# Kernel optimization log

Hardware: AMD Instinct MI355X
Metric: run time of the kernel (lower is better)

The kernel has to match this reference:

```python
import jax, jax.numpy as jnp
import numpy as np

EPS = 1e-5

def _bn(y, g, b):
    # BatchNorm1d training-mode math: biased batch stats over (batch, spatial)
    m = jnp.mean(y, axis=(0, 2), keepdims=True)
    v = jnp.var(y, axis=(0, 2), keepdims=True)
    return (y - m) / jnp.sqrt(v + EPS) * g[None, :, None] + b[None, :, None]

def setup_inputs() -> dict:
    key = jax.random.key(0)
    ks = jax.random.split(key, 8)
    B, C, HW = 32, 512, 1024
    D = C // 8
    s = 0.02
    return {
        "x": jax.random.normal(ks[0], (B, C, HW), dtype=jnp.float32),
        "bn1_g": jnp.ones((C,), jnp.float32),
        "bn1_b": jnp.zeros((C,), jnp.float32),
        "W_qkv": jax.random.normal(ks[1], (2 * D + C, C), jnp.float32) * s,
        "b_qkv": jnp.zeros((2 * D + C,), jnp.float32),
        "bn2_g": jnp.ones((C,), jnp.float32),
        "bn2_b": jnp.zeros((C,), jnp.float32),
        "W1": jax.random.normal(ks[2], (C, C), jnp.float32) * s,
        "b1": jnp.zeros((C,), jnp.float32),
        "W2": jax.random.normal(ks[3], (C, C), jnp.float32) * s,
        "b2": jnp.zeros((C,), jnp.float32),
    }

def reference(x, bn1_g, bn1_b, W_qkv, b_qkv, bn2_g, bn2_b, W1, b1, W2, b2):
    b, c, hw = x.shape
    d = c // 8
    h = jax.nn.relu(_bn(x, bn1_g, bn1_b))
    # 1x1 conv == channel matmul: [b, 2d+c, hw]
    qkv = jnp.einsum('oc,bch->boh', W_qkv, h) + b_qkv[None, :, None]
    q, k, v = qkv[:, :d], qkv[:, d:2 * d], qkv[:, 2 * d:]
    # beta[b, q_pos, k_pos]; note softmax over axis=1 (query axis), per original
    beta = jnp.einsum('bdq,bdk->bqk', q, k) / jnp.sqrt(jnp.asarray(d, x.dtype))
    beta = jax.nn.softmax(beta, axis=1)
    att = jnp.einsum('bcq,bqk->bck', v, beta)  # [b, c, hw]
    xr = x + att
    y = _bn(xr, bn2_g, bn2_b)
    y = jnp.transpose(y, (0, 2, 1))  # [b, hw, c]
    y = jax.nn.relu(y @ W1.T + b1) @ W2.T + b2
    return xr + jnp.transpose(y, (0, 2, 1))
```

## Files before the change

kernel.cpp:

```cpp
#include <hip/hip_runtime.h>

#define BB 32
#define CC 512
#define HWN 1024
#define DD 64
#define OO 640

typedef short bf16x8 __attribute__((ext_vector_type(8)));
typedef float f32x4 __attribute__((ext_vector_type(4)));
typedef __attribute__((address_space(1))) const void gvoid;
typedef __attribute__((address_space(3))) void svoid;

__device__ __forceinline__ void gload_lds16(const void* g, void* l) {
    __builtin_amdgcn_global_load_lds((gvoid*)g, (svoid*)l, 16, 0, 0);
}

__device__ __forceinline__ unsigned short f2bf(float f) {
    unsigned int u = __float_as_uint(f);
    unsigned int r = u + 0x7FFFu + ((u >> 16) & 1u);
    return (unsigned short)(r >> 16);
}
__device__ __forceinline__ float bf2f(unsigned short h) {
    return __uint_as_float(((unsigned int)h) << 16);
}

__global__ __launch_bounds__(256) void cvt3_kernel(const float* __restrict__ a,
                                                   const float* __restrict__ b,
                                                   const float* __restrict__ c,
                                                   unsigned short* __restrict__ oa,
                                                   unsigned short* __restrict__ ob,
                                                   unsigned short* __restrict__ oc) {
    const int n1 = OO * CC, n2 = CC * CC;
    int i = blockIdx.x * 256 + threadIdx.x;
    if (i < n1)            oa[i] = f2bf(a[i]);
    else if (i < n1 + n2)  ob[i - n1] = f2bf(b[i - n1]);
    else                   oc[i - n1 - n2] = f2bf(c[i - n1 - n2]);
}

template <bool INBF16>
__global__ __launch_bounds__(256) void bn_stats_kernel(const void* __restrict__ xv,
                                                       float* __restrict__ mean,
                                                       float* __restrict__ rstd) {
    int c = blockIdx.x;
    int t = threadIdx.x;
    float s = 0.f, s2 = 0.f;
    if (INBF16) {
        const unsigned int* x = (const unsigned int*)xv;
        for (int b = 0; b < BB; ++b) {
            const unsigned int* p = x + ((size_t)b * CC + c) * (HWN / 2);
#pragma unroll
            for (int i = 0; i < 2; ++i) {
                unsigned int w = p[t + i * 256];
                float v0 = bf2f((unsigned short)(w & 0xffffu));
                float v1 = bf2f((unsigned short)(w >> 16));
                s += v0 + v1; s2 += v0 * v0 + v1 * v1;
            }
        }
    } else {
        const float* x = (const float*)xv;
        for (int b = 0; b < BB; ++b) {
            const float* p = x + ((size_t)b * CC + c) * HWN;
#pragma unroll
            for (int i = 0; i < 4; ++i) {
                float v = p[t + i * 256];
                s += v; s2 += v * v;
            }
        }
    }
    for (int off = 32; off > 0; off >>= 1) {
        s  += __shfl_down(s,  off, 64);
        s2 += __shfl_down(s2, off, 64);
    }
    __shared__ float sh[4], sh2[4];
    int wave = t >> 6;
    if ((t & 63) == 0) { sh[wave] = s; sh2[wave] = s2; }
    __syncthreads();
    if (t == 0) {
        float ts = 0.f, ts2 = 0.f;
        for (int w = 0; w < 4; ++w) { ts += sh[w]; ts2 += sh2[w]; }
        const float invN = 1.f / (float)(BB * HWN);
        float m = ts * invN;
        float var = ts2 * invN - m * m;
        mean[c] = m;
        rstd[c] = rsqrtf(var + 1e-5f);
    }
}

template <bool RELU, bool INBF16>
__global__ __launch_bounds__(256) void bn_apply_t_kernel(const void* __restrict__ xv,
                                                         const float* __restrict__ mean,
                                                         const float* __restrict__ rstd,
                                                         const float* __restrict__ g,
                                                         const float* __restrict__ bta,
                                                         unsigned short* __restrict__ outT) {
    __shared__ float tile[64][65];
    int b  = blockIdx.z;
    int c0 = blockIdx.y * 64;
    int s0 = blockIdx.x * 64;
    int t = threadIdx.x;
    int sl = t & 63, grp = t >> 6;
#pragma unroll
    for (int i = 0; i < 16; ++i) {
        int cr = i * 4 + grp;
        int c = c0 + cr;
        float r  = rstd[c] * g[c];
        float sh = bta[c] - mean[c] * r;
        float xval;
        if (INBF16) {
            const unsigned short* xb = (const unsigned short*)xv;
            xval = bf2f(xb[((size_t)b * CC + c0 + cr) * HWN + s0 + sl]);
        } else {
            const float* xb = (const float*)xv;
            xval = xb[((size_t)b * CC + c0 + cr) * HWN + s0 + sl];
        }
        float v = fmaf(xval, r, sh);
        if (RELU) v = fmaxf(v, 0.f);
        tile[cr][sl] = v;
    }
    __syncthreads();
    unsigned short* ob = outT + ((size_t)b * HWN + s0) * CC + c0;
#pragma unroll
    for (int i = 0; i < 16; ++i) {
        int srow = i * 4 + grp;
        ob[(size_t)srow * CC + sl] = f2bf(tile[sl][srow]);
    }
}

__global__ __launch_bounds__(256) void reduce_bnstats_kernel(const float* __restrict__ part,
                                                             float* __restrict__ mean,
                                                             float* __restrict__ rstd) {
    int c = blockIdx.x * 256 + threadIdx.x;
    float s = 0.f, s2 = 0.f;
    for (int p = 0; p < BB * 8; ++p) {
        s  += part[(size_t)p * 1024 + c];
        s2 += part[(size_t)p * 1024 + 512 + c];
    }
    const float invN = 1.f / (float)(BB * HWN);
    float m = s * invN;
    mean[c] = m;
    rstd[c] = rsqrtf(s2 * invN - m * m + 1e-5f);
}

__global__ __launch_bounds__(512, 2) void fused_pv_kernel(
        const unsigned short* __restrict__ qkTg,
        const unsigned short* __restrict__ vg,
        const float* __restrict__ xg,
        unsigned short* __restrict__ xrg,
        float* __restrict__ rowpart) {
    __shared__ __align__(16) unsigned short Ks[2 * 128 * 32];
    __shared__ __align__(16) unsigned short Qs[2][2 * 64 * 32];
    __shared__ __align__(16) unsigned short Vs[2 * 512 * 32];
    __shared__ __align__(16) unsigned short Es[2 * 128 * 32];
    __shared__ float sS[128];
    __shared__ float rsS[2][512];
    __shared__ float rqS[2][512];

    int b = blockIdx.z;
    int n0 = blockIdx.x * 128;
    const unsigned short* qk = qkTg + (size_t)b * (HWN * 128);
    const unsigned short* vb = vg + (size_t)b * ((size_t)CC * HWN);
    int t = threadIdx.x;
    int wv = t >> 6, L = t & 63;
    int lr = L & 15, lq = L >> 4;
    int swz = (lr >> 1) & 3;
    int cstrip = (wv >> 1) * 128;
    int khalf = (wv & 1) * 64;

#pragma unroll
    for (int is = 0; is < 2; ++is) {
        int idx = is * 512 + t;
        int kkd = idx >> 9, row = (idx >> 2) & 127, slot = idx & 3;
        int ch = slot ^ ((row >> 1) & 3);
        gload_lds16(qk + (size_t)(n0 + row) * 128 + 64 + kkd * 32 + ch * 8, &Ks[idx * 8]);
    }
    {
        int kkd = t >> 8, row = (t >> 2) & 63, slot = t & 3;
        int ch = slot ^ ((row >> 1) & 3);
        gload_lds16(qk + (size_t)row * 128 + kkd * 32 + ch * 8, &Qs[0][t * 8]);
    }

    f32x4 acc[8][4] = {};
    float S = 0.f;
    int p = 0;
    for (int i = 0; i < 16; ++i) {
        int q0 = i * 64;
#pragma unroll
        for (int is = 0; is < 8; ++is) {
            int idx = is * 512 + t;
            int kkq = idx >> 11, row = (idx >> 2) & 511, slot = idx & 3;
            int ch = slot ^ ((row >> 1) & 3);
            gload_lds16(vb + (size_t)row * HWN + q0 + kkq * 32 + ch * 8, &Vs[idx * 8]);
        }
        if (i + 1 < 16) {
            int kkd = t >> 8, row = (t >> 2) & 63, slot = t & 3;
            int ch = slot ^ ((row >> 1) & 3);
            gload_lds16(qk + (size_t)(q0 + 64 + row) * 128 + kkd * 32 + ch * 8,
                        &Qs[p ^ 1][t * 8]);
        }
        if (i == 0) __syncthreads();

        f32x4 eacc[4] = {};
#pragma unroll
        for (int kkd = 0; kkd < 2; ++kkd) {
            bf16x8 kb = *(const bf16x8*)&Ks[kkd * 4096 + (wv * 16 + lr) * 32 + ((lq ^ swz) * 8)];
#pragma unroll
            for (int qi = 0; qi < 4; ++qi) {
                bf16x8 qa = *(const bf16x8*)&Qs[p][kkd * 2048 + (qi * 16 + lr) * 32 + ((lq ^ swz) * 8)];
                eacc[qi] = __builtin_amdgcn_mfma_f32_16x16x32_bf16(qa, kb, eacc[qi], 0, 0, 0);
            }
        }
        float spart = 0.f;
#pragma unroll
        for (int qi = 0; qi < 4; ++qi) {
            float e0 = __expf(eacc[qi][0] * 0.125f);
            float e1 = __expf(eacc[qi][1] * 0.125f);
            float e2 = __expf(eacc[qi][2] * 0.125f);
            float e3 = __expf(eacc[qi][3] * 0.125f);
            spart += (e0 + e1) + (e2 + e3);
            unsigned int lo = (unsigned int)f2bf(e0) | ((unsigned int)f2bf(e1) << 16);
            unsigned int hi = (unsigned int)f2bf(e2) | ((unsigned int)f2bf(e3) << 16);
            int kkq = qi >> 1;
            int chunkE = (qi & 1) * 2 + (lq >> 1);
            int addr = kkq * 4096 + (wv * 16 + lr) * 32 + ((chunkE ^ swz) * 8) + (lq & 1) * 4;
            *(uint2*)&Es[addr] = make_uint2(lo, hi);
        }
        spart += __shfl_xor(spart, 16, 64);
        spart += __shfl_xor(spart, 32, 64);
        S += spart;
        __syncthreads();

#pragma unroll
        for (int kk = 0; kk < 2; ++kk) {
            bf16x8 af[8], bfj[4];
#pragma unroll
            for (int ii = 0; ii < 8; ++ii)
                af[ii] = *(const bf16x8*)&Vs[kk * 16384 + (cstrip + ii * 16 + lr) * 32 + ((lq ^ swz) * 8)];
#pragma unroll
            for (int j = 0; j < 4; ++j)
                bfj[j] = *(const bf16x8*)&Es[kk * 4096 + (khalf + j * 16 + lr) * 32 + ((lq ^ swz) * 8)];
#pragma unroll
            for (int ii = 0; ii < 8; ++ii)
#pragma unroll
                for (int j = 0; j < 4; ++j)
                    acc[ii][j] = __builtin_amdgcn_mfma_f32_16x16x32_bf16(af[ii], bfj[j], acc[ii][j], 0, 0, 0);
        }
        __syncthreads();
        p ^= 1;
    }

    if (lq == 0) sS[wv * 16 + lr] = S;
    __syncthreads();
    float inv[4];
#pragma unroll
    for (int j = 0; j < 4; ++j) inv[j] = 1.f / sS[khalf + j * 16 + lr];

    const float* xb = xg + (size_t)b * ((size_t)CC * HWN);
    unsigned short* xrb = xrg + (size_t)b * ((size_t)CC * HWN);
#pragma unroll
    for (int ii = 0; ii < 8; ++ii) {
#pragma unroll
        for (int r = 0; r < 4; ++r) {
            int row = cstrip + ii * 16 + lq * 4 + r;
            float s = 0.f, q2 = 0.f;
#pragma unroll
            for (int j = 0; j < 4; ++j) {
                int col = n0 + khalf + j * 16 + lr;
                float val = acc[ii][j][r] * inv[j];
                size_t off = (size_t)row * HWN + col;
                val += xb[off];
                s += val; q2 += val * val;
                xrb[off] = f2bf(val);
            }
#pragma unroll
            for (int m = 1; m <= 8; m <<= 1) {
                s += __shfl_xor(s, m, 64);
                q2 += __shfl_xor(q2, m, 64);
            }
            if (lr == 0) { rsS[wv & 1][row] = s; rqS[wv & 1][row] = q2; }
        }
    }
    __syncthreads();
    {
        size_t base = ((size_t)b * 8 + blockIdx.x) * 1024;
        rowpart[base + t] = rsS[0][t] + rsS[1][t];
        rowpart[base + 512 + t] = rqS[0][t] + rqS[1][t];
    }
}

template <bool OUTBF16, int BIASMODE , bool RELU,
          int RESMODE >
__global__ __launch_bounds__(256, 4) void mfma_gemm(const unsigned short* __restrict__ A,
                                                 const unsigned short* __restrict__ Bt,
                                                 const float* __restrict__ bias,
                                                 const void* __restrict__ resid,
                                                 void* __restrict__ C,
                                                 int K, int lda, int ldb, int ldc,
                                                 long strideA, long strideB, long strideC,
                                                 float scale) {
    __shared__ __align__(16) unsigned short As[2][128 * 32];
    __shared__ __align__(16) unsigned short Bs[2][128 * 32];
    int b  = blockIdx.z;
    int m0 = blockIdx.y * 128;
    int n0 = blockIdx.x * 128;
    const unsigned short* Ab = A  + (size_t)b * strideA;
    const unsigned short* Bb = Bt + (size_t)b * strideB;
    int t = threadIdx.x;
    int wv = t >> 6, L = t & 63;
    int wm = (wv >> 1) * 64, wn = (wv & 1) * 64;
    int lr = L & 15, lq = L >> 4;
    int srow = t >> 2;
    int gchunk = (t & 3) ^ ((t >> 3) & 3);
    int skof = gchunk * 8;
    int swz = (lr >> 1) & 3;

    int aoff[4], boff[4];
#pragma unroll
    for (int i = 0; i < 4; ++i) {
        aoff[i] = (wm + i * 16 + lr) * 32 + ((lq ^ swz) * 8);
        boff[i] = (wn + i * 16 + lr) * 32 + ((lq ^ swz) * 8);
    }

    const unsigned short* gA0 = Ab + (size_t)(m0 + srow) * lda + skof;
    const unsigned short* gA1 = Ab + (size_t)(m0 + 64 + srow) * lda + skof;
    const unsigned short* gB0 = Bb + (size_t)(n0 + srow) * ldb + skof;
    const unsigned short* gB1 = Bb + (size_t)(n0 + 64 + srow) * ldb + skof;

    f32x4 acc[4][4] = {};
    int nIter = K >> 5;

    gload_lds16(gA0, &As[0][t * 8]);
    gload_lds16(gA1, &As[0][64 * 32 + t * 8]);
    gload_lds16(gB0, &Bs[0][t * 8]);
    gload_lds16(gB1, &Bs[0][64 * 32 + t * 8]);

    int p = 0;
    for (int i = 0; i < nIter; ++i) {
        __syncthreads();
        if (i + 1 < nIter) {
            int ko = (i + 1) << 5;
            gload_lds16(gA0 + ko, &As[p ^ 1][t * 8]);
            gload_lds16(gA1 + ko, &As[p ^ 1][64 * 32 + t * 8]);
            gload_lds16(gB0 + ko, &Bs[p ^ 1][t * 8]);
            gload_lds16(gB1 + ko, &Bs[p ^ 1][64 * 32 + t * 8]);
        }
        bf16x8 af[4], bfr[4];
#pragma unroll
        for (int j = 0; j < 4; ++j) af[j]  = *(const bf16x8*)&As[p][aoff[j]];
#pragma unroll
        for (int j = 0; j < 4; ++j) bfr[j] = *(const bf16x8*)&Bs[p][boff[j]];
#pragma unroll
        for (int ii = 0; ii < 4; ++ii)
#pragma unroll
            for (int jj = 0; jj < 4; ++jj)
                acc[ii][jj] = __builtin_amdgcn_mfma_f32_16x16x32_bf16(af[ii], bfr[jj], acc[ii][jj], 0, 0, 0);
        p ^= 1;
    }

#pragma unroll
    for (int i = 0; i < 4; ++i) {
#pragma unroll
        for (int r = 0; r < 4; ++r) {
            int row = m0 + wm + i * 16 + lq * 4 + r;
            float brow = (BIASMODE == 1) ? bias[row] : 0.f;
#pragma unroll
            for (int j = 0; j < 4; ++j) {
                int col = n0 + wn + j * 16 + lr;
                float v = acc[i][j][r] * scale;
                if (BIASMODE == 1) v += brow;
                if (BIASMODE == 2) v += bias[col];
                if (RELU) v = fmaxf(v, 0.f);
                size_t off = (size_t)b * strideC + (size_t)row * ldc + col;
                if (RESMODE == 1) v += ((const float*)resid)[off];
                if (RESMODE == 2) v += bf2f(((const unsigned short*)resid)[off]);
                if (OUTBF16) ((unsigned short*)C)[off] = f2bf(v);
                else         ((float*)C)[off] = v;
            }
        }
    }
}

extern "C" void kernel_launch(void* const* d_in, const int* in_sizes, int n_in,
                              void* d_out, int out_size, void* d_ws, size_t ws_size,
                              hipStream_t stream) {
    const float* x     = (const float*)d_in[0];
    const float* bn1_g = (const float*)d_in[1];
    const float* bn1_b = (const float*)d_in[2];
    const float* W_qkv = (const float*)d_in[3];
    const float* b_qkv = (const float*)d_in[4];
    const float* bn2_g = (const float*)d_in[5];
    const float* bn2_b = (const float*)d_in[6];
    const float* W1    = (const float*)d_in[7];
    const float* b1    = (const float*)d_in[8];
    const float* W2    = (const float*)d_in[9];
    const float* b2    = (const float*)d_in[10];
    float* out = (float*)d_out;
    char* ws = (char*)d_ws;

    unsigned short* hT    = (unsigned short*)(ws);
    unsigned short* qkT   = (unsigned short*)(ws + 33554432);
    unsigned short* v     = (unsigned short*)(ws + 41943040);
    unsigned short* xr    = (unsigned short*)(ws + 142606336);
    unsigned short* Wqkvb = (unsigned short*)(ws + 176160768);
    unsigned short* W1b   = (unsigned short*)(ws + 176816128);
    unsigned short* W2b   = (unsigned short*)(ws + 177340416);
    float* stats = (float*)(ws + 177864704);
    float* mean1 = stats,        *rstd1 = stats + 512;
    float* mean2 = stats + 1024, *rstd2 = stats + 1536;
    unsigned short* ybnT = hT;
    unsigned short* y1T  = v;
    float* rowpartBN = (float*)(ws + 1179648);

    const long sHT = (long)HWN * CC;
    const long sQK = (long)HWN * 128;
    const long sV  = (long)CC * HWN;

    cvt3_kernel<<<(OO * CC + 2 * CC * CC) / 256, 256, 0, stream>>>(W_qkv, W1, W2, Wqkvb, W1b, W2b);
    bn_stats_kernel<false><<<CC, 256, 0, stream>>>(x, mean1, rstd1);
    bn_apply_t_kernel<true, false><<<dim3(16, 8, BB), 256, 0, stream>>>(x, mean1, rstd1, bn1_g, bn1_b, hT);
    mfma_gemm<true, 2, false, 0><<<dim3(1, 8, BB), 256, 0, stream>>>(
        hT, Wqkvb, b_qkv, nullptr, qkT, 512, 512, 512, 128, sHT, 0, sQK, 1.f);
    mfma_gemm<true, 1, false, 0><<<dim3(8, 4, BB), 256, 0, stream>>>(
        Wqkvb + 128 * 512, hT, b_qkv + 128, nullptr, v, 512, 512, 512, 1024, 0, sHT, sV, 1.f);
    fused_pv_kernel<<<dim3(8, 1, BB), 512, 0, stream>>>(qkT, v, x, xr, rowpartBN);
    reduce_bnstats_kernel<<<2, 256, 0, stream>>>(rowpartBN, mean2, rstd2);
    bn_apply_t_kernel<false, true><<<dim3(16, 8, BB), 256, 0, stream>>>(xr, mean2, rstd2, bn2_g, bn2_b, ybnT);
    mfma_gemm<true, 2, true, 0><<<dim3(4, 8, BB), 256, 0, stream>>>(
        ybnT, W1b, b1, nullptr, y1T, 512, 512, 512, 512, sHT, 0, sHT, 1.f);
    mfma_gemm<false, 1, false, 2><<<dim3(8, 4, BB), 256, 0, stream>>>(
        W2b, y1T, b2, xr, out, 512, 512, 512, 1024, 0, sHT, sV, 1.f);
}
```

Before: 376.6 us.

## Split fused PV kernel over channel halves to double grid size and occupancy

The fused softmax-PV kernel now splits the 512 value channels into two 256-channel halves per block, doubling the grid from 256 to 512 blocks. This halves the V tile, the accumulator registers and the LDS footprint, and raises launch bounds to 4 blocks per CU. The Q tile is now single-buffered and its prefetch is issued after the barrier. In exchange, each half recomputes the QK^T exponentials, doubling that work, and it loses the overlap that double-buffered Q gave.

```diff
diff --git a/kernel.cpp b/kernel.cpp
--- a/kernel.cpp
+++ b/kernel.cpp
@@ -141,61 +141,58 @@
     rstd[c] = rsqrtf(s2 * invN - m * m + 1e-5f);
 }
 
-__global__ __launch_bounds__(512, 2) void fused_pv_kernel(
+__global__ __launch_bounds__(512, 4) void fused_pv_kernel(
         const unsigned short* __restrict__ qkTg,
         const unsigned short* __restrict__ vg,
         const float* __restrict__ xg,
         unsigned short* __restrict__ xrg,
         float* __restrict__ rowpart) {
     __shared__ __align__(16) unsigned short Ks[2 * 128 * 32];
-    __shared__ __align__(16) unsigned short Qs[2][2 * 64 * 32];
-    __shared__ __align__(16) unsigned short Vs[2 * 512 * 32];
+    __shared__ __align__(16) unsigned short Qs[2 * 64 * 32];
+    __shared__ __align__(16) unsigned short Vs[2 * 256 * 32];
     __shared__ __align__(16) unsigned short Es[2 * 128 * 32];
     __shared__ float sS[128];
-    __shared__ float rsS[2][512];
-    __shared__ float rqS[2][512];
-
-    int b = blockIdx.z;
-    int n0 = blockIdx.x * 128;
+    __shared__ float rsS[2][256];
+    __shared__ float rqS[2][256];
+
+    int lin = blockIdx.x + 16 * blockIdx.z;
+    int b  = lin & 31;
+    int nn = (lin >> 5) & 7;
+    int ch = lin >> 8;
+    int n0 = nn * 128;
+    int c0 = ch * 256;
     const unsigned short* qk = qkTg + (size_t)b * (HWN * 128);
     const unsigned short* vb = vg + (size_t)b * ((size_t)CC * HWN);
     int t = threadIdx.x;
     int wv = t >> 6, L = t & 63;
     int lr = L & 15, lq = L >> 4;
     int swz = (lr >> 1) & 3;
-    int cstrip = (wv >> 1) * 128;
+    int cstrip = (wv >> 1) * 64;
     int khalf = (wv & 1) * 64;
 
 #pragma unroll
     for (int is = 0; is < 2; ++is) {
         int idx = is * 512 + t;
         int kkd = idx >> 9, row = (idx >> 2) & 127, slot = idx & 3;
-        int ch = slot ^ ((row >> 1) & 3);
-        gload_lds16(qk + (size_t)(n0 + row) * 128 + 64 + kkd * 32 + ch * 8, &Ks[idx * 8]);
+        int chk = slot ^ ((row >> 1) & 3);
+        gload_lds16(qk + (size_t)(n0 + row) * 128 + 64 + kkd * 32 + chk * 8, &Ks[idx * 8]);
     }
     {
         int kkd = t >> 8, row = (t >> 2) & 63, slot = t & 3;
-        int ch = slot ^ ((row >> 1) & 3);
-        gload_lds16(qk + (size_t)row * 128 + kkd * 32 + ch * 8, &Qs[0][t * 8]);
-    }
-
-    f32x4 acc[8][4] = {};
+        int chk = slot ^ ((row >> 1) & 3);
+        gload_lds16(qk + (size_t)row * 128 + kkd * 32 + chk * 8, &Qs[t * 8]);
+    }
+
+    f32x4 acc[4][4] = {};
     float S = 0.f;
-    int p = 0;
     for (int i = 0; i < 16; ++i) {
         int q0 = i * 64;
 #pragma unroll
-        for (int is = 0; is < 8; ++is) {
+        for (int is = 0; is < 4; ++is) {
             int idx = is * 512 + t;
-            int kkq = idx >> 11, row = (idx >> 2) & 511, slot = idx & 3;
-            int ch = slot ^ ((row >> 1) & 3);
-            gload_lds16(vb + (size_t)row * HWN + q0 + kkq * 32 + ch * 8, &Vs[idx * 8]);
-        }
-        if (i + 1 < 16) {
-            int kkd = t >> 8, row = (t >> 2) & 63, slot = t & 3;
-            int ch = slot ^ ((row >> 1) & 3);
-            gload_lds16(qk + (size_t)(q0 + 64 + row) * 128 + kkd * 32 + ch * 8,
-                        &Qs[p ^ 1][t * 8]);
+            int kkq = idx >> 10, row = (idx >> 2) & 255, slot = idx & 3;
+            int chk = slot ^ ((row >> 1) & 3);
+            gload_lds16(vb + (size_t)(c0 + row) * HWN + q0 + kkq * 32 + chk * 8, &Vs[idx * 8]);
         }
         if (i == 0) __syncthreads();
 
@@ -205,7 +202,7 @@
             bf16x8 kb = *(const bf16x8*)&Ks[kkd * 4096 + (wv * 16 + lr) * 32 + ((lq ^ swz) * 8)];
 #pragma unroll
             for (int qi = 0; qi < 4; ++qi) {
-                bf16x8 qa = *(const bf16x8*)&Qs[p][kkd * 2048 + (qi * 16 + lr) * 32 + ((lq ^ swz) * 8)];
+                bf16x8 qa = *(const bf16x8*)&Qs[kkd * 2048 + (qi * 16 + lr) * 32 + ((lq ^ swz) * 8)];
                 eacc[qi] = __builtin_amdgcn_mfma_f32_16x16x32_bf16(qa, kb, eacc[qi], 0, 0, 0);
             }
         }
@@ -229,23 +226,28 @@
         S += spart;
         __syncthreads();
 
+        if (i + 1 < 16) {
+            int kkd = t >> 8, row = (t >> 2) & 63, slot = t & 3;
+            int chk = slot ^ ((row >> 1) & 3);
+            gload_lds16(qk + (size_t)(q0 + 64 + row) * 128 + kkd * 32 + chk * 8, &Qs[t * 8]);
+        }
+
 #pragma unroll
         for (int kk = 0; kk < 2; ++kk) {
-            bf16x8 af[8], bfj[4];
-#pragma unroll
-            for (int ii = 0; ii < 8; ++ii)
-                af[ii] = *(const bf16x8*)&Vs[kk * 16384 + (cstrip + ii * 16 + lr) * 32 + ((lq ^ swz) * 8)];
+            bf16x8 af[4], bfj[4];
+#pragma unroll
+            for (int ii = 0; ii < 4; ++ii)
+                af[ii] = *(const bf16x8*)&Vs[kk * 8192 + (cstrip + ii * 16 + lr) * 32 + ((lq ^ swz) * 8)];
 #pragma unroll
             for (int j = 0; j < 4; ++j)
                 bfj[j] = *(const bf16x8*)&Es[kk * 4096 + (khalf + j * 16 + lr) * 32 + ((lq ^ swz) * 8)];
 #pragma unroll
-            for (int ii = 0; ii < 8; ++ii)
+            for (int ii = 0; ii < 4; ++ii)
 #pragma unroll
                 for (int j = 0; j < 4; ++j)
                     acc[ii][j] = __builtin_amdgcn_mfma_f32_16x16x32_bf16(af[ii], bfj[j], acc[ii][j], 0, 0, 0);
         }
         __syncthreads();
-        p ^= 1;
     }
 
     if (lq == 0) sS[wv * 16 + lr] = S;
@@ -257,10 +259,11 @@
     const float* xb = xg + (size_t)b * ((size_t)CC * HWN);
     unsigned short* xrb = xrg + (size_t)b * ((size_t)CC * HWN);
 #pragma unroll
-    for (int ii = 0; ii < 8; ++ii) {
+    for (int ii = 0; ii < 4; ++ii) {
 #pragma unroll
         for (int r = 0; r < 4; ++r) {
-            int row = cstrip + ii * 16 + lq * 4 + r;
+            int rloc = cstrip + ii * 16 + lq * 4 + r;
+            int row = c0 + rloc;
             float s = 0.f, q2 = 0.f;
 #pragma unroll
             for (int j = 0; j < 4; ++j) {
@@ -276,14 +279,15 @@
                 s += __shfl_xor(s, m, 64);
                 q2 += __shfl_xor(q2, m, 64);
             }
-            if (lr == 0) { rsS[wv & 1][row] = s; rqS[wv & 1][row] = q2; }
+            if (lr == 0) { rsS[wv & 1][rloc] = s; rqS[wv & 1][rloc] = q2; }
         }
     }
     __syncthreads();
     {
-        size_t base = ((size_t)b * 8 + blockIdx.x) * 1024;
-        rowpart[base + t] = rsS[0][t] + rsS[1][t];
-        rowpart[base + 512 + t] = rqS[0][t] + rqS[1][t];
+        size_t base = ((size_t)b * 8 + nn) * 1024;
+        int rloc = t & 255;
+        if (t < 256) rowpart[base + c0 + rloc]       = rsS[0][rloc] + rsS[1][rloc];
+        else         rowpart[base + 512 + c0 + rloc] = rqS[0][rloc] + rqS[1][rloc];
     }
 }
 
@@ -421,7 +425,7 @@
         hT, Wqkvb, b_qkv, nullptr, qkT, 512, 512, 512, 128, sHT, 0, sQK, 1.f);
     mfma_gemm<true, 1, false, 0><<<dim3(8, 4, BB), 256, 0, stream>>>(
         Wqkvb + 128 * 512, hT, b_qkv + 128, nullptr, v, 512, 512, 512, 1024, 0, sHT, sV, 1.f);
-    fused_pv_kernel<<<dim3(8, 1, BB), 512, 0, stream>>>(qkT, v, x, xr, rowpartBN);
+    fused_pv_kernel<<<dim3(16, 1, BB), 512, 0, stream>>>(qkT, v, x, xr, rowpartBN);
     reduce_bnstats_kernel<<<2, 256, 0, stream>>>(rowpartBN, mean2, rstd2);
     bn_apply_t_kernel<false, true><<<dim3(16, 8, BB), 256, 0, stream>>>(xr, mean2, rstd2, bn2_g, bn2_b, ybnT);
     mfma_gemm<true, 2, true, 0><<<dim3(4, 8, BB), 256, 0, stream>>>(
```

After: 366.4 us. 1.03x faster.
